# Performance work log

Hardware: AMD Instinct MI355X
Metric: run time of the kernel (lower is better)

Reference implementation:

```python
import jax, jax.numpy as jnp
import numpy as np

B, S, H = 1, 2048, 4096
NH, NKV, D = 32, 8, 128
ROPE_THETA = 10000.0


def _rotate_half(x):
    half = x.shape[-1] // 2
    return jnp.concatenate([-x[..., half:], x[..., :half]], axis=-1)


def _rope_cos_sin(position_ids, dim, theta):
    inv_freq = 1.0 / (theta ** (jnp.arange(0, dim, 2, dtype=jnp.float32) / dim))  # [D/2]
    freqs = position_ids.astype(jnp.float32)[..., None] * inv_freq  # [B,S,D/2]
    emb = jnp.concatenate([freqs, freqs], axis=-1)  # [B,S,D]
    return jnp.cos(emb)[:, None], jnp.sin(emb)[:, None]  # [B,1,S,D]


def setup_inputs() -> dict:
    key = jax.random.key(0)
    k1, k2, k3 = jax.random.split(key, 3)
    hidden_states = jax.random.normal(k1, (B, S, H), dtype=jnp.float32)
    # fused QKV weight: columns = [NH*D | NKV*D | NKV*D]
    w_qkv = jax.random.normal(k2, (H, (NH + 2 * NKV) * D), dtype=jnp.float32) * (1.0 / np.sqrt(H))
    w_o = jax.random.normal(k3, (NH * D, H), dtype=jnp.float32) * (1.0 / np.sqrt(NH * D))
    attention_mask = jnp.tril(jnp.ones((S, S), dtype=bool))[None, None]  # causal [1,1,S,S]
    position_ids = jnp.arange(S, dtype=jnp.int64 if jax.config.jax_enable_x64 else jnp.int32)[None, :]
    return {"hidden_states": hidden_states, "w_qkv": w_qkv, "w_o": w_o,
            "attention_mask": attention_mask, "position_ids": position_ids}


def reference(hidden_states, w_qkv, w_o, attention_mask, position_ids):
    bsz, q_len, _ = hidden_states.shape
    qk_scale = 1.0 / np.sqrt(D)

    # fused QKV projection
    qkv = jnp.einsum('bsh,hc->bsc', hidden_states, w_qkv)
    q = qkv[..., : NH * D].reshape(bsz, q_len, NH, D).transpose(0, 2, 1, 3)        # [B,NH,S,D]
    k = qkv[..., NH * D: (NH + NKV) * D].reshape(bsz, q_len, NKV, D).transpose(0, 2, 1, 3)
    v = qkv[..., (NH + NKV) * D:].reshape(bsz, q_len, NKV, D).transpose(0, 2, 1, 3)

    # RoPE
    cos, sin = _rope_cos_sin(position_ids, D, ROPE_THETA)
    q = q * cos + _rotate_half(q) * sin
    k = k * cos + _rotate_half(k) * sin

    # GQA expand kv heads
    groups = NH // NKV
    k = jnp.repeat(k, groups, axis=1)  # [B,NH,S,D]
    v = jnp.repeat(v, groups, axis=1)

    # causal masked attention (eager path, matches scaled_qk + softmax(fp32))
    scores = jnp.einsum('bhqd,bhkd->bhqk', q, k) * qk_scale
    scores = jnp.where(attention_mask, scores, jnp.finfo(scores.dtype).min)
    probs = jax.nn.softmax(scores.astype(jnp.float32), axis=-1).astype(q.dtype)
    attn = jnp.einsum('bhqk,bhkd->bhqd', probs, v)  # [B,NH,S,D]

    # merge heads + output projection
    attn = attn.transpose(0, 2, 1, 3).reshape(bsz, q_len, NH * D)
    return jnp.einsum('bsd,dh->bsh', attn, w_o)
```

## Files before the change

kernel.cpp:

```cpp
#include <hip/hip_runtime.h>
#include <cstdint>
#include <cstddef>


#define DEV __device__ __forceinline__

typedef __attribute__((ext_vector_type(4))) float  f32x4;
typedef __attribute__((ext_vector_type(4))) short  short4v;
typedef __attribute__((ext_vector_type(8))) short  short8;
typedef __attribute__((ext_vector_type(8))) __bf16 bf16x8;

DEV short f32_to_bf16(float x) {
  union { float f; uint32_t u; } v; v.f = x;
  uint32_t r = v.u + 0x7fffu + ((v.u >> 16) & 1u);
  return (short)(r >> 16);
}

union frag_u { short4v h[2]; bf16x8 v; short s[8]; uint32_t u[4]; };
DEV bf16x8 comb(short4v lo, short4v hi) { frag_u u; u.h[0] = lo; u.h[1] = hi; return u.v; }

DEV uint32_t pack2bf_trunc(float a, float b) {
  union { float f; uint32_t u; } x, y; x.f = a; y.f = b;
  return (x.u >> 16) | (y.u & 0xFFFF0000u);
}

DEV f32x4 MFMA(bf16x8 a, bf16x8 b, f32x4 c) {
  return __builtin_amdgcn_mfma_f32_16x16x32_bf16(a, b, c, 0, 0, 0);
}

typedef __attribute__((address_space(1))) void* gas1p;
typedef __attribute__((address_space(3))) void* as3p;
DEV void gld16(const void* g, void* l) {
  __builtin_amdgcn_global_load_lds((gas1p)g, (as3p)l, 16, 0, 0);
}

#define VMCNT(n) asm volatile("s_waitcnt vmcnt(" #n ")" ::: "memory")


__global__ __launch_bounds__(256) void k_cvt_bf16(const float* __restrict__ x,
                                                  short* __restrict__ y, int n4) {
  int i = blockIdx.x * 256 + threadIdx.x;
  int stride = gridDim.x * 256;
  for (; i < n4; i += stride) {
    f32x4 v = ((const f32x4*)x)[i];
    short4v o;
    o[0] = f32_to_bf16(v[0]); o[1] = f32_to_bf16(v[1]);
    o[2] = f32_to_bf16(v[2]); o[3] = f32_to_bf16(v[3]);
    ((short4v*)y)[i] = o;
  }
}

__global__ __launch_bounds__(256) void k_transpose64(const float* __restrict__ src,
                                                     short* __restrict__ dst,
                                                     int R, int C, int stride) {
  __shared__ float tile[64][65];
  const int c0 = blockIdx.x * 64, r0 = blockIdx.y * 64;
  const int t = threadIdx.x;
  const int lr = t >> 4;
  const int lc = (t & 15) * 4;
  #pragma unroll
  for (int p = 0; p < 4; ++p) {
    const int r = p * 16 + lr;
    f32x4 v = *(const f32x4*)(src + (long)(r0 + r) * stride + c0 + lc);
    tile[r][lc] = v[0]; tile[r][lc + 1] = v[1]; tile[r][lc + 2] = v[2]; tile[r][lc + 3] = v[3];
  }
  __syncthreads();
  #pragma unroll
  for (int p = 0; p < 4; ++p) {
    const int c = p * 16 + lr;
    short4v o;
    o[0] = f32_to_bf16(tile[lc][c]);     o[1] = f32_to_bf16(tile[lc + 1][c]);
    o[2] = f32_to_bf16(tile[lc + 2][c]); o[3] = f32_to_bf16(tile[lc + 3][c]);
    *(short4v*)(dst + (long)(c0 + c) * R + r0 + lc) = o;
  }
}

__global__ __launch_bounds__(256) void k_vtrans64(const float* __restrict__ C1,
                                                  short* __restrict__ Vt) {
  __shared__ float tile[64][65];
  const int s0 = blockIdx.x * 64, d0 = blockIdx.y * 64, z = blockIdx.z;
  const int t = threadIdx.x;
  const int lr = t >> 4;
  const int lc = (t & 15) * 4;
  const float* src = C1 + 5120 + z * 128;
  #pragma unroll
  for (int p = 0; p < 4; ++p) {
    const int r = p * 16 + lr;
    f32x4 v = *(const f32x4*)(src + (long)(s0 + r) * 6144 + d0 + lc);
    tile[r][lc] = v[0]; tile[r][lc + 1] = v[1]; tile[r][lc + 2] = v[2]; tile[r][lc + 3] = v[3];
  }
  __syncthreads();
  short* dst = Vt + (long)z * 128 * 2048;
  const int pb = 32 * ((lc >> 5) & 1) + 8 * ((lc >> 2) & 3) + 4 * ((lc >> 4) & 1);
  #pragma unroll
  for (int p = 0; p < 4; ++p) {
    const int d = p * 16 + lr;
    short4v o;
    o[0] = f32_to_bf16(tile[lc][d]);     o[1] = f32_to_bf16(tile[lc + 1][d]);
    o[2] = f32_to_bf16(tile[lc + 2][d]); o[3] = f32_to_bf16(tile[lc + 3][d]);
    *(short4v*)(dst + (long)(d0 + d) * 2048 + s0 + pb) = o;
  }
}

__global__ __launch_bounds__(256) void k_rope_pack(const float* __restrict__ C1,
                                                   short* __restrict__ Qh,
                                                   short* __restrict__ Kh) {
  __shared__ float cs[64], sn[64];
  const int s = blockIdx.x, t = threadIdx.x;
  if (t < 64) {
    float inv = powf(10000.0f, -(float)t * (1.0f / 64.0f));
    float a = (float)s * inv;
    cs[t] = cosf(a);
    sn[t] = sinf(a);
  }
  __syncthreads();
  const float* row = C1 + (long)s * 6144;
  #pragma unroll
  for (int wv = 0; wv < 2; ++wv) {
    const int base = t + wv * 256;
    const int hh = base >> 4, jq = (base & 15) * 4;
    f32x4 c  = *(const f32x4*)&cs[jq];
    f32x4 sv = *(const f32x4*)&sn[jq];
    f32x4 x0 = *(const f32x4*)(row + hh * 128 + jq);
    f32x4 x1 = *(const f32x4*)(row + hh * 128 + jq + 64);
    const long o = ((long)hh * 2048 + s) * 128 + jq;
    short4v lo_, hi_;
    #pragma unroll
    for (int e = 0; e < 4; ++e) {
      lo_[e] = f32_to_bf16(x0[e] * c[e] - x1[e] * sv[e]);
      hi_[e] = f32_to_bf16(x1[e] * c[e] + x0[e] * sv[e]);
    }
    *(short4v*)(Qh + o)      = lo_;
    *(short4v*)(Qh + o + 64) = hi_;
  }
  if (t < 128) {
    const int hh = t >> 4, jq = (t & 15) * 4;
    f32x4 c  = *(const f32x4*)&cs[jq];
    f32x4 sv = *(const f32x4*)&sn[jq];
    f32x4 x0 = *(const f32x4*)(row + 4096 + hh * 128 + jq);
    f32x4 x1 = *(const f32x4*)(row + 4096 + hh * 128 + jq + 64);
    const long o = ((long)hh * 2048 + s) * 128 + jq;
    short4v lo_, hi_;
    #pragma unroll
    for (int e = 0; e < 4; ++e) {
      lo_[e] = f32_to_bf16(x0[e] * c[e] - x1[e] * sv[e]);
      hi_[e] = f32_to_bf16(x1[e] * c[e] + x0[e] * sv[e]);
    }
    *(short4v*)(Kh + o)      = lo_;
    *(short4v*)(Kh + o + 64) = hi_;
  }
}


template<int MR>
DEV void gemm8p_engine(const short* __restrict__ A, const short* __restrict__ Bt,
                       float* __restrict__ Cp, int N, int K,
                       char* __restrict__ AsB, char* __restrict__ BsB) {
  constexpr int BM = MR * 32;
  const int tid = threadIdx.x;
  const int lane = tid & 63;
  const int w = tid >> 6;
  const int wm = w >> 2, wn = w & 3;
  const int wr = wm * (MR * 16);
  const int wc = wn * 64;
  const int g = lane >> 4, r16 = lane & 15;
  const long m0 = (long)blockIdx.y * BM;
  const long n0 = (long)blockIdx.x * 256;
  const int l8 = lane >> 3, l7 = lane & 7;
  const int sslot = l7 ^ l8;

  f32x4 acc[MR][4] = {};
  const int NT = K >> 6;

  auto stageA = [&](int h, int kt, int bufn) {
    #pragma unroll
    for (int s = 0; s < BM / 128; ++s) {
      const int rb = h * (BM / 2) + s * 64 + w * 8;
      gld16(A + (m0 + rb + l8) * (long)K + kt * 64 + sslot * 8,
            AsB + ((size_t)bufn * BM + rb) * 128);
    }
  };
  auto stageB = [&](int h, int kt, int bufn) {
    #pragma unroll
    for (int s = 0; s < 2; ++s) {
      const int rb = h * 128 + s * 64 + w * 8;
      gld16(Bt + (n0 + rb + l8) * (long)K + kt * 64 + sslot * 8,
            BsB + ((size_t)bufn * 256 + rb) * 128);
    }
  };

  bf16x8 a[MR / 2][2], b0[2][2], b1[2][2];

  #define LDA_HALF(h, buf) { _Pragma("unroll") for (int m = 0; m < MR/2; ++m) \
      _Pragma("unroll") for (int kk = 0; kk < 2; ++kk) { \
        const int row = wr + ((h) * (MR/2) + m) * 16 + r16; \
        const int slot = ((kk << 2) | g) ^ (r16 & 7); \
        a[m][kk] = *(const bf16x8*)(AsB + ((size_t)(buf) * BM + row) * 128 + slot * 16); } }
  #define LDB_HALF(dst, h, buf) { _Pragma("unroll") for (int n = 0; n < 2; ++n) \
      _Pragma("unroll") for (int kk = 0; kk < 2; ++kk) { \
        const int row = wc + ((h) * 2 + n) * 16 + r16; \
        const int slot = ((kk << 2) | g) ^ (r16 & 7); \
        dst[n][kk] = *(const bf16x8*)(BsB + ((size_t)(buf) * 256 + row) * 128 + slot * 16); } }
  #define QUADQ(mh, nh, bb) { __builtin_amdgcn_s_setprio(1); \
      _Pragma("unroll") for (int m = 0; m < MR/2; ++m) \
      _Pragma("unroll") for (int n = 0; n < 2; ++n) \
      _Pragma("unroll") for (int kk = 0; kk < 2; ++kk) \
        acc[(mh) * (MR/2) + m][(nh) * 2 + n] = \
          MFMA(a[m][kk], bb[n][kk], acc[(mh) * (MR/2) + m][(nh) * 2 + n]); \
      __builtin_amdgcn_s_setprio(0); }

  stageA(0, 0, 0); stageB(0, 0, 0); stageB(1, 0, 0); stageA(1, 0, 0);
  VMCNT(4);
  __builtin_amdgcn_s_barrier();

  for (int t = 0; t < NT - 1; ++t) {
    const int buf = t & 1, bufn = buf ^ 1, tn = t + 1;
    LDA_HALF(0, buf); LDB_HALF(b0, 0, buf);
    stageA(0, tn, bufn);
    __builtin_amdgcn_s_barrier();
    QUADQ(0, 0, b0);
    VMCNT(4);
    __builtin_amdgcn_s_barrier();
    LDB_HALF(b1, 1, buf);
    stageB(0, tn, bufn);
    __builtin_amdgcn_s_barrier();
    QUADQ(0, 1, b1);
    VMCNT(4);
    __builtin_amdgcn_s_barrier();
    LDA_HALF(1, buf);
    stageB(1, tn, bufn);
    __builtin_amdgcn_s_barrier();
    QUADQ(1, 1, b1);
    __builtin_amdgcn_s_barrier();
    stageA(1, tn, bufn);
    QUADQ(1, 0, b0);
    VMCNT(4);
    __builtin_amdgcn_s_barrier();
  }
  {
    const int buf = (NT - 1) & 1;
    LDA_HALF(0, buf); LDB_HALF(b0, 0, buf);
    __builtin_amdgcn_s_barrier();
    QUADQ(0, 0, b0);
    VMCNT(2);
    __builtin_amdgcn_s_barrier();
    LDB_HALF(b1, 1, buf);
    __builtin_amdgcn_s_barrier();
    QUADQ(0, 1, b1);
    VMCNT(0);
    __builtin_amdgcn_s_barrier();
    LDA_HALF(1, buf);
    __builtin_amdgcn_s_barrier();
    QUADQ(1, 1, b1);
    QUADQ(1, 0, b0);
  }
  #undef LDA_HALF
  #undef LDB_HALF
  #undef QUADQ

  #pragma unroll
  for (int m = 0; m < MR; ++m) {
    #pragma unroll
    for (int n = 0; n < 4; ++n) {
      const long col = n0 + wc + n * 16 + r16;
      #pragma unroll
      for (int j = 0; j < 4; ++j) {
        const long row = m0 + wr + m * 16 + g * 4 + j;
        Cp[row * N + col] = acc[m][n][j];
      }
    }
  }
}

__global__ __launch_bounds__(512, 2) void k_gemm1_8p(const short* __restrict__ A,
                                                     const short* __restrict__ Bt,
                                                     float* __restrict__ C, int N, int K) {
  __shared__ short As[2][256][64];
  __shared__ short Bs[2][256][64];
  gemm8p_engine<8>(A, Bt, C, N, K, (char*)&As[0][0][0], (char*)&Bs[0][0][0]);
}


template<int OUT_BF16>
__global__ __launch_bounds__(256, 2) void k_gemm128(const short* __restrict__ A,
                                                    const short* __restrict__ Bt,
                                                    void* __restrict__ Cp,
                                                    int M, int N, int K) {
  __shared__ short As[2][128][64];
  __shared__ short Bs[2][128][64];
  const int tid = threadIdx.x;
  const int lane = tid & 63;
  const int w = tid >> 6;
  const int wr = (w >> 1) * 64;
  const int wc = (w & 1) * 64;
  const int g = lane >> 4, r16 = lane & 15;
  const long m0 = (long)blockIdx.y * 128;
  const long n0 = (long)blockIdx.x * 128;
  const int l8 = lane >> 3, l7 = lane & 7;
  const int sslot = l7 ^ l8;

  f32x4 acc[4][4] = {};
  const int NT = K >> 6;

  auto stageTile = [&](int kt, int buf) {
    #pragma unroll
    for (int L = 0; L < 4; ++L) {
      const int rb = (w * 4 + L) * 8;
      gld16(A  + (m0 + rb + l8) * (long)K + kt * 64 + sslot * 8, (char*)&As[buf][rb][0]);
      gld16(Bt + (n0 + rb + l8) * (long)K + kt * 64 + sslot * 8, (char*)&Bs[buf][rb][0]);
    }
  };
  auto ldA = [&](int m, int kk, int buf) -> bf16x8 {
    const int row = wr + m * 16 + r16;
    const int slot = ((kk << 2) | g) ^ (r16 & 7);
    return *(const bf16x8*)((const char*)&As[buf][0][0] + row * 128 + slot * 16);
  };
  auto ldB = [&](int n, int kk, int buf) -> bf16x8 {
    const int row = wc + n * 16 + r16;
    const int slot = ((kk << 2) | g) ^ (r16 & 7);
    return *(const bf16x8*)((const char*)&Bs[buf][0][0] + row * 128 + slot * 16);
  };

  stageTile(0, 0);
  __syncthreads();

  for (int t = 0; t < NT; ++t) {
    const int buf = t & 1;
    if (t + 1 < NT) stageTile(t + 1, buf ^ 1);

    bf16x8 a[2][2], b[2][2];
    #pragma unroll
    for (int mh = 0; mh < 2; ++mh) {
      #pragma unroll
      for (int m = 0; m < 2; ++m)
        #pragma unroll
        for (int kk = 0; kk < 2; ++kk) a[m][kk] = ldA(mh * 2 + m, kk, buf);
      #pragma unroll
      for (int nh = 0; nh < 2; ++nh) {
        #pragma unroll
        for (int n = 0; n < 2; ++n)
          #pragma unroll
          for (int kk = 0; kk < 2; ++kk) b[n][kk] = ldB(nh * 2 + n, kk, buf);
        #pragma unroll
        for (int m = 0; m < 2; ++m)
          #pragma unroll
          for (int n = 0; n < 2; ++n)
            #pragma unroll
            for (int kk = 0; kk < 2; ++kk)
              acc[mh * 2 + m][nh * 2 + n] =
                MFMA(a[m][kk], b[n][kk], acc[mh * 2 + m][nh * 2 + n]);
      }
    }
    __syncthreads();
  }

  #pragma unroll
  for (int m = 0; m < 4; ++m) {
    #pragma unroll
    for (int n = 0; n < 4; ++n) {
      const long col = n0 + wc + n * 16 + r16;
      #pragma unroll
      for (int j = 0; j < 4; ++j) {
        const long row = m0 + wr + m * 16 + g * 4 + j;
        if (OUT_BF16) ((short*)Cp)[row * N + col] = f32_to_bf16(acc[m][n][j]);
        else          ((float*)Cp)[row * N + col] = acc[m][n][j];
      }
    }
  }
}


__global__ __launch_bounds__(256, 2) void k_attn(const short* __restrict__ Qh,
                                                 const short* __restrict__ Kh,
                                                 const short* __restrict__ Vt,
                                                 short* __restrict__ O) {
  __shared__ short Kl[64][128];
  __shared__ short Vl[128][64];
  const int h = blockIdx.x, by = blockIdx.y, hk = h >> 2;
  const int qt = (by < 8) ? (2 * by) : (15 - 2 * (by - 8));
  const int tid = threadIdx.x, lane = tid & 63, w = tid >> 6;
  const int g = lane >> 4, r16 = lane & 15;
  const int q0w = qt * 128 + w * 32;

  bf16x8 qf[2][4];
  #pragma unroll
  for (int qb = 0; qb < 2; ++qb) {
    const short* qb_ptr = Qh + ((long)h * 2048 + q0w + qb * 16 + r16) * 128;
    #pragma unroll
    for (int c = 0; c < 4; ++c)
      qf[qb][c] = *(const bf16x8*)(qb_ptr + 32 * c + 8 * g);
  }
  const short* Kg = Kh + (long)hk * (2048 * 128);
  const short* Vg = Vt + (long)hk * (128 * 2048);

  f32x4 accO[2][8] = {};
  float mrun[2] = {-1e30f, -1e30f}, lrun[2] = {0.0f, 0.0f};
  const int NTB = 2 * qt + 2;

  short8 kpre[4], vpre[4];
  #pragma unroll
  for (int j = 0; j < 4; ++j) {
    const int n = tid + j * 256;
    kpre[j] = *(const short8*)(Kg + ((long)(n >> 4)) * 128 + (n & 15) * 8);
    vpre[j] = *(const short8*)(Vg + (long)(n >> 3) * 2048 + (n & 7) * 8);
  }

  for (int kt = 0; kt < NTB; ++kt) {
    #pragma unroll
    for (int j = 0; j < 4; ++j) {
      const int n = tid + j * 256;
      const int krow = n >> 4, kslot = n & 15;
      *(short8*)((char*)&Kl[0][0] + krow * 256 + ((kslot ^ (krow & 7)) * 16)) = kpre[j];
      const int vrow = n >> 3, vslot = n & 7;
      *(short8*)((char*)&Vl[0][0] + vrow * 128 + ((vslot ^ (vrow & 7)) * 16)) = vpre[j];
    }
    __syncthreads();

    if (kt + 1 < NTB) {
      const long koff = (long)(kt + 1) * 64;
      #pragma unroll
      for (int j = 0; j < 4; ++j) {
        const int n = tid + j * 256;
        kpre[j] = *(const short8*)(Kg + (koff + (n >> 4)) * 128 + (n & 15) * 8);
        vpre[j] = *(const short8*)(Vg + (long)(n >> 3) * 2048 + koff + (n & 7) * 8);
      }
    }

    if (kt * 64 <= q0w + 31) {
      f32x4 accS[2][4] = {};
      __builtin_amdgcn_s_setprio(1);
      #pragma unroll
      for (int kvf = 0; kvf < 4; ++kvf) {
        const char* krB = (const char*)&Kl[0][0] + (kvf * 16 + r16) * 256;
        const int rx = r16 & 7;
        #pragma unroll
        for (int c = 0; c < 4; ++c) {
          bf16x8 af = *(const bf16x8*)(krB + (((c << 2) | g) ^ rx) * 16);
          accS[0][kvf] = MFMA(af, qf[0][c], accS[0][kvf]);
          accS[1][kvf] = MFMA(af, qf[1][c], accS[1][kvf]);
        }
      }
      __builtin_amdgcn_s_setprio(0);

      const bool diag = (kt * 64 + 63 > q0w);
      frag_u p0[2], p1[2];
      #pragma unroll
      for (int qb = 0; qb < 2; ++qb) {
        const int q_glob = q0w + qb * 16 + r16;
        float sc[4][4];
        #pragma unroll
        for (int kvf = 0; kvf < 4; ++kvf)
          #pragma unroll
          for (int r = 0; r < 4; ++r) sc[kvf][r] = accS[qb][kvf][r] * 0.08838834764831845f;
        if (diag) {
          #pragma unroll
          for (int kvf = 0; kvf < 4; ++kvf)
            #pragma unroll
            for (int r = 0; r < 4; ++r) {
              const int kvg = kt * 64 + kvf * 16 + g * 4 + r;
              if (kvg > q_glob) sc[kvf][r] = -1e30f;
            }
        }
        float rm[4];
        #pragma unroll
        for (int kvf = 0; kvf < 4; ++kvf)
          rm[kvf] = fmaxf(fmaxf(sc[kvf][0], sc[kvf][1]), fmaxf(sc[kvf][2], sc[kvf][3]));
        float mt = fmaxf(fmaxf(rm[0], rm[1]), fmaxf(rm[2], rm[3]));
        mt = fmaxf(mt, __shfl_xor(mt, 16));
        mt = fmaxf(mt, __shfl_xor(mt, 32));

        const bool nonew = __all(mt <= mrun[qb]);
        const float mnew = nonew ? mrun[qb] : fmaxf(mrun[qb], mt);
        float pk[4];
        #pragma unroll
        for (int kvf = 0; kvf < 4; ++kvf) {
          #pragma unroll
          for (int r = 0; r < 4; ++r) sc[kvf][r] = __expf(sc[kvf][r] - mnew);
          pk[kvf] = (sc[kvf][0] + sc[kvf][1]) + (sc[kvf][2] + sc[kvf][3]);
        }
        float ps = (pk[0] + pk[1]) + (pk[2] + pk[3]);
        ps += __shfl_xor(ps, 16);
        ps += __shfl_xor(ps, 32);
        if (nonew) {
          lrun[qb] += ps;
        } else {
          const float scale = __expf(mrun[qb] - mnew);
          lrun[qb] = lrun[qb] * scale + ps;
          mrun[qb] = mnew;
          #pragma unroll
          for (int df = 0; df < 8; ++df)
            #pragma unroll
            for (int j = 0; j < 4; ++j) accO[qb][df][j] *= scale;
        }
        p0[qb].u[0] = pack2bf_trunc(sc[0][0], sc[0][1]);
        p0[qb].u[1] = pack2bf_trunc(sc[0][2], sc[0][3]);
        p0[qb].u[2] = pack2bf_trunc(sc[1][0], sc[1][1]);
        p0[qb].u[3] = pack2bf_trunc(sc[1][2], sc[1][3]);
        p1[qb].u[0] = pack2bf_trunc(sc[2][0], sc[2][1]);
        p1[qb].u[1] = pack2bf_trunc(sc[2][2], sc[2][3]);
        p1[qb].u[2] = pack2bf_trunc(sc[3][0], sc[3][1]);
        p1[qb].u[3] = pack2bf_trunc(sc[3][2], sc[3][3]);
      }

      __builtin_amdgcn_s_setprio(1);
      #pragma unroll
      for (int df = 0; df < 8; ++df) {
        const int d = df * 16 + r16;
        const char* vrB = (const char*)&Vl[0][0] + d * 128;
        const int rx = d & 7;
        bf16x8 v01 = *(const bf16x8*)(vrB + ((g ^ rx) * 16));
        bf16x8 v23 = *(const bf16x8*)(vrB + (((4 + g) ^ rx) * 16));
        accO[0][df] = MFMA(v01, p0[0].v, accO[0][df]);
        accO[0][df] = MFMA(v23, p1[0].v, accO[0][df]);
        accO[1][df] = MFMA(v01, p0[1].v, accO[1][df]);
        accO[1][df] = MFMA(v23, p1[1].v, accO[1][df]);
      }
      __builtin_amdgcn_s_setprio(0);
    }
    __syncthreads();
  }

  #pragma unroll
  for (int qb = 0; qb < 2; ++qb) {
    const int q_glob = q0w + qb * 16 + r16;
    const float invl = 1.0f / lrun[qb];
    #pragma unroll
    for (int df = 0; df < 8; ++df) {
      const int d0 = df * 16 + g * 4;
      short4v o;
      #pragma unroll
      for (int j = 0; j < 4; ++j) o[j] = f32_to_bf16(accO[qb][df][j] * invl);
      *(short4v*)(O + (long)q_glob * 4096 + h * 128 + d0) = o;
    }
  }
}


extern "C" void kernel_launch(void* const* d_in, const int* in_sizes, int n_in,
                              void* d_out, int out_size, void* d_ws, size_t ws_size,
                              hipStream_t stream) {
  const float* hs   = (const float*)d_in[0];
  const float* wqkv = (const float*)d_in[1];
  const float* wo   = (const float*)d_in[2];

  const size_t OFF_HSB = 0;
  const size_t OFF_W1T = 16777216;
  const size_t OFF_WOT = 67108864;
  const size_t OFF_C1  = 100663296;
  const size_t OFF_KH  = 152043520;
  const size_t OFF_VT  = 156237824;
  if (ws_size < 160432128u) return;

  char* ws = (char*)d_ws;
  short* hsb = (short*)(ws + OFF_HSB);
  short* W1T = (short*)(ws + OFF_W1T);
  short* WoT = (short*)(ws + OFF_WOT);
  float* C1  = (float*)(ws + OFF_C1);
  short* Kh  = (short*)(ws + OFF_KH);
  short* Vt  = (short*)(ws + OFF_VT);
  short* Qh  = hsb;
  short* AO  = (short*)(ws + OFF_C1);

  k_cvt_bf16<<<2048, 256, 0, stream>>>(hs, hsb, 2048 * 4096 / 4);
  k_transpose64<<<dim3(96, 64), 256, 0, stream>>>(wqkv, W1T, 4096, 6144, 6144);
  k_transpose64<<<dim3(64, 64), 256, 0, stream>>>(wo, WoT, 4096, 4096, 4096);
  k_gemm1_8p<<<dim3(24, 8), 512, 0, stream>>>(hsb, W1T, C1, 6144, 4096);
  k_rope_pack<<<2048, 256, 0, stream>>>(C1, Qh, Kh);
  k_vtrans64<<<dim3(32, 2, 8), 256, 0, stream>>>(C1, Vt);
  k_attn<<<dim3(32, 16), 256, 0, stream>>>(Qh, Kh, Vt, AO);
  k_gemm128<0><<<dim3(32, 16), 256, 0, stream>>>(AO, WoT, (void*)d_out, 2048, 4096, 4096);
}
```

Before: 336.3 us.

## Replace output-projection GEMM with 256x128-tile, 8-wave, phased-pipeline kernel

The output projection GEMM moves from a 128x128 tile with 4 waves to a 256x128 tile with 8 waves. The K loop is split into four quadrant phases, and loads of the next tile's A/B halves are interleaved with MFMA quadrants using explicit vmcnt waits, barriers and setprio. This mirrors the 8-phase engine already used for the QKV GEMM, aiming for better overlap of global loads with MFMA and more A reuse. In exchange the grid shrinks to 256 blocks, which may underfill the GPU's CUs, and the hand-tuned synchronisation is fragile.

```diff
diff --git a/kernel.cpp b/kernel.cpp
--- a/kernel.cpp
+++ b/kernel.cpp
@@ -281,20 +281,20 @@
 }
 
 
-template<int OUT_BF16>
-__global__ __launch_bounds__(256, 2) void k_gemm128(const short* __restrict__ A,
-                                                    const short* __restrict__ Bt,
-                                                    void* __restrict__ Cp,
-                                                    int M, int N, int K) {
-  __shared__ short As[2][128][64];
+__global__ __launch_bounds__(512, 2) void k_gemm2_bn128(const short* __restrict__ A,
+                                                        const short* __restrict__ Bt,
+                                                        float* __restrict__ Cp,
+                                                        int N, int K) {
+  __shared__ short As[2][256][64];
   __shared__ short Bs[2][128][64];
   const int tid = threadIdx.x;
   const int lane = tid & 63;
   const int w = tid >> 6;
-  const int wr = (w >> 1) * 64;
-  const int wc = (w & 1) * 64;
+  const int wm = w >> 1, wn = w & 1;
+  const int wr = wm * 64;
+  const int wc = wn * 64;
   const int g = lane >> 4, r16 = lane & 15;
-  const long m0 = (long)blockIdx.y * 128;
+  const long m0 = (long)blockIdx.y * 256;
   const long n0 = (long)blockIdx.x * 128;
   const int l8 = lane >> 3, l7 = lane & 7;
   const int sslot = l7 ^ l8;
@@ -302,57 +302,88 @@
   f32x4 acc[4][4] = {};
   const int NT = K >> 6;
 
-  auto stageTile = [&](int kt, int buf) {
-    #pragma unroll
-    for (int L = 0; L < 4; ++L) {
-      const int rb = (w * 4 + L) * 8;
-      gld16(A  + (m0 + rb + l8) * (long)K + kt * 64 + sslot * 8, (char*)&As[buf][rb][0]);
-      gld16(Bt + (n0 + rb + l8) * (long)K + kt * 64 + sslot * 8, (char*)&Bs[buf][rb][0]);
+  auto stageA = [&](int h, int kt, int bufn) {
+    #pragma unroll
+    for (int s = 0; s < 2; ++s) {
+      const int rb = h * 128 + s * 64 + w * 8;
+      gld16(A + (m0 + rb + l8) * (long)K + kt * 64 + sslot * 8,
+            (char*)&As[bufn][rb][0]);
     }
   };
-  auto ldA = [&](int m, int kk, int buf) -> bf16x8 {
-    const int row = wr + m * 16 + r16;
-    const int slot = ((kk << 2) | g) ^ (r16 & 7);
-    return *(const bf16x8*)((const char*)&As[buf][0][0] + row * 128 + slot * 16);
+  auto stageB = [&](int h, int kt, int bufn) {
+    const int rb = h * 64 + w * 8;
+    gld16(Bt + (n0 + rb + l8) * (long)K + kt * 64 + sslot * 8,
+          (char*)&Bs[bufn][rb][0]);
   };
-  auto ldB = [&](int n, int kk, int buf) -> bf16x8 {
-    const int row = wc + n * 16 + r16;
-    const int slot = ((kk << 2) | g) ^ (r16 & 7);
-    return *(const bf16x8*)((const char*)&Bs[buf][0][0] + row * 128 + slot * 16);
-  };
-
-  stageTile(0, 0);
-  __syncthreads();
-
-  for (int t = 0; t < NT; ++t) {
-    const int buf = t & 1;
-    if (t + 1 < NT) stageTile(t + 1, buf ^ 1);
-
-    bf16x8 a[2][2], b[2][2];
-    #pragma unroll
-    for (int mh = 0; mh < 2; ++mh) {
-      #pragma unroll
-      for (int m = 0; m < 2; ++m)
-        #pragma unroll
-        for (int kk = 0; kk < 2; ++kk) a[m][kk] = ldA(mh * 2 + m, kk, buf);
-      #pragma unroll
-      for (int nh = 0; nh < 2; ++nh) {
-        #pragma unroll
-        for (int n = 0; n < 2; ++n)
-          #pragma unroll
-          for (int kk = 0; kk < 2; ++kk) b[n][kk] = ldB(nh * 2 + n, kk, buf);
-        #pragma unroll
-        for (int m = 0; m < 2; ++m)
-          #pragma unroll
-          for (int n = 0; n < 2; ++n)
-            #pragma unroll
-            for (int kk = 0; kk < 2; ++kk)
-              acc[mh * 2 + m][nh * 2 + n] =
-                MFMA(a[m][kk], b[n][kk], acc[mh * 2 + m][nh * 2 + n]);
-      }
-    }
-    __syncthreads();
-  }
+
+  bf16x8 a[2][2], b0[2][2], b1[2][2];
+
+  #define LDA_HALF2(mh, buf) { _Pragma("unroll") for (int m = 0; m < 2; ++m) \
+      _Pragma("unroll") for (int kk = 0; kk < 2; ++kk) { \
+        const int row = wr + ((mh) * 2 + m) * 16 + r16; \
+        const int slot = ((kk << 2) | g) ^ (r16 & 7); \
+        a[m][kk] = *(const bf16x8*)((const char*)&As[buf][0][0] + row * 128 + slot * 16); } }
+  #define LDB_HALF2(dst, nh, buf) { _Pragma("unroll") for (int n = 0; n < 2; ++n) \
+      _Pragma("unroll") for (int kk = 0; kk < 2; ++kk) { \
+        const int row = wc + ((nh) * 2 + n) * 16 + r16; \
+        const int slot = ((kk << 2) | g) ^ (r16 & 7); \
+        dst[n][kk] = *(const bf16x8*)((const char*)&Bs[buf][0][0] + row * 128 + slot * 16); } }
+  #define QUADQ2(mh, nh, bb) { __builtin_amdgcn_s_setprio(1); \
+      _Pragma("unroll") for (int m = 0; m < 2; ++m) \
+      _Pragma("unroll") for (int n = 0; n < 2; ++n) \
+      _Pragma("unroll") for (int kk = 0; kk < 2; ++kk) \
+        acc[(mh) * 2 + m][(nh) * 2 + n] = \
+          MFMA(a[m][kk], bb[n][kk], acc[(mh) * 2 + m][(nh) * 2 + n]); \
+      __builtin_amdgcn_s_setprio(0); }
+
+  stageA(0, 0, 0); stageB(0, 0, 0); stageB(1, 0, 0); stageA(1, 0, 0);
+  VMCNT(3);
+  __builtin_amdgcn_s_barrier();
+
+  for (int t = 0; t < NT - 1; ++t) {
+    const int buf = t & 1, bufn = buf ^ 1, tn = t + 1;
+    LDA_HALF2(0, buf); LDB_HALF2(b0, 0, buf);
+    stageA(0, tn, bufn);
+    __builtin_amdgcn_s_barrier();
+    QUADQ2(0, 0, b0);
+    VMCNT(4);
+    __builtin_amdgcn_s_barrier();
+    LDB_HALF2(b1, 1, buf);
+    stageB(0, tn, bufn);
+    __builtin_amdgcn_s_barrier();
+    QUADQ2(0, 1, b1);
+    VMCNT(3);
+    __builtin_amdgcn_s_barrier();
+    LDA_HALF2(1, buf);
+    stageB(1, tn, bufn);
+    __builtin_amdgcn_s_barrier();
+    QUADQ2(1, 1, b1);
+    __builtin_amdgcn_s_barrier();
+    stageA(1, tn, bufn);
+    QUADQ2(1, 0, b0);
+    VMCNT(3);
+    __builtin_amdgcn_s_barrier();
+  }
+  {
+    const int buf = (NT - 1) & 1;
+    LDA_HALF2(0, buf); LDB_HALF2(b0, 0, buf);
+    __builtin_amdgcn_s_barrier();
+    QUADQ2(0, 0, b0);
+    VMCNT(2);
+    __builtin_amdgcn_s_barrier();
+    LDB_HALF2(b1, 1, buf);
+    __builtin_amdgcn_s_barrier();
+    QUADQ2(0, 1, b1);
+    VMCNT(0);
+    __builtin_amdgcn_s_barrier();
+    LDA_HALF2(1, buf);
+    __builtin_amdgcn_s_barrier();
+    QUADQ2(1, 1, b1);
+    QUADQ2(1, 0, b0);
+  }
+  #undef LDA_HALF2
+  #undef LDB_HALF2
+  #undef QUADQ2
 
   #pragma unroll
   for (int m = 0; m < 4; ++m) {
@@ -362,8 +393,7 @@
       #pragma unroll
       for (int j = 0; j < 4; ++j) {
         const long row = m0 + wr + m * 16 + g * 4 + j;
-        if (OUT_BF16) ((short*)Cp)[row * N + col] = f32_to_bf16(acc[m][n][j]);
-        else          ((float*)Cp)[row * N + col] = acc[m][n][j];
+        Cp[row * N + col] = acc[m][n][j];
       }
     }
   }
@@ -568,5 +598,5 @@
   k_rope_pack<<<2048, 256, 0, stream>>>(C1, Qh, Kh);
   k_vtrans64<<<dim3(32, 2, 8), 256, 0, stream>>>(C1, Vt);
   k_attn<<<dim3(32, 16), 256, 0, stream>>>(Qh, Kh, Vt, AO);
-  k_gemm128<0><<<dim3(32, 16), 256, 0, stream>>>(AO, WoT, (void*)d_out, 2048, 4096, 4096);
-}
+  k_gemm2_bn128<<<dim3(32, 8), 512, 0, stream>>>(AO, WoT, (float*)d_out, 4096, 4096);
+}
```

Measured after the change: 346.9 us. 1.03x slower.
